# Kernel optimization log

Measured on AMD Instinct MI355X. Metric: run time of the kernel, lower is better.

The kernel has to match this reference:

```python
import jax, jax.numpy as jnp
import numpy as np

DIM_IN, DIM_K, DIM_V = 1024, 1024, 1024

def setup_inputs() -> dict:
    key = jax.random.key(0)
    k1, k2, k3, k4 = jax.random.split(key, 4)
    x = jax.random.normal(k1, (4, 2048, DIM_IN), dtype=jnp.float32)
    # Linear(dim_in, dim_k, bias=False): store as [in, out] for x @ W
    Wq = jax.random.normal(k2, (DIM_IN, DIM_K), dtype=jnp.float32) * (1.0 / np.sqrt(DIM_IN))
    Wk = jax.random.normal(k3, (DIM_IN, DIM_K), dtype=jnp.float32) * (1.0 / np.sqrt(DIM_IN))
    Wv = jax.random.normal(k4, (DIM_IN, DIM_V), dtype=jnp.float32) * (1.0 / np.sqrt(DIM_IN))
    return {"x": x, "Wq": Wq, "Wk": Wk, "Wv": Wv, "causal_mask": 1}

def reference(x, Wq, Wk, Wv, causal_mask):
    # x: [b, n, dim_in]
    b, n, _ = x.shape
    q = jnp.einsum('bnd,dk->bnk', x, Wq)
    k = jnp.einsum('bnd,dk->bnk', x, Wk)
    v = jnp.einsum('bnd,dv->bnv', x, Wv)
    scale = 1.0 / np.sqrt(Wq.shape[1])
    dist = jnp.einsum('bik,bjk->bij', q, k) * scale  # [b, n, n]
    if causal_mask:
        mask = jnp.tril(jnp.ones((n, n), dtype=bool))
        dist = jnp.where(mask, dist, -jnp.inf)
    attn = jax.nn.softmax(dist, axis=-1)
    return jnp.einsum('bij,bjv->biv', attn, v)  # [b, n, dim_v]
```

## Files before the change

kernel.cpp:

```cpp
#include <hip/hip_runtime.h>
#include <hip/hip_bf16.h>
#include <stdint.h>

#define BM 128
#define BN 128
#define BK 64

typedef __attribute__((ext_vector_type(8))) short bf16x8;
typedef __attribute__((ext_vector_type(4))) float floatx4;


__device__ __forceinline__ unsigned short f2bf(float f) {
    unsigned int x;
    __builtin_memcpy(&x, &f, 4);
    unsigned int r = (x + 0x7fffu + ((x >> 16) & 1u)) >> 16;
    return (unsigned short)r;
}

__device__ __forceinline__ float bf2f_hi(unsigned int u_hi_masked) {
    float f;
    __builtin_memcpy(&f, &u_hi_masked, 4);
    return f;
}

__device__ __forceinline__ void async_copy16(const void* g, void* l) {
    __builtin_amdgcn_global_load_lds(
        (const __attribute__((address_space(1))) void*)(uintptr_t)g,
        (__attribute__((address_space(3))) void*)(uint32_t)(uintptr_t)l,
        16, 0, 0);
}


__global__ __launch_bounds__(256) void prep(const float* __restrict__ x,
                                            const float* __restrict__ Wq,
                                            const float* __restrict__ Wk,
                                            const float* __restrict__ Wv,
                                            unsigned short* __restrict__ xb,
                                            unsigned short* __restrict__ wT) {
    __shared__ float tile[32][33];
    int bid = blockIdx.x;
    int tid = threadIdx.x;
    if (bid < 8192) {
        int i = bid * 256 + tid;
        float4 v = ((const float4*)x)[i];
        ushort4 o;
        o.x = f2bf(v.x);
        o.y = f2bf(v.y);
        o.z = f2bf(v.z);
        o.w = f2bf(v.w);
        ((ushort4*)xb)[i] = o;
    } else {
        int w = bid - 8192;
        int z = w >> 10;
        int r = w & 1023;
        int bx = (r & 31) * 32;
        int by = (r >> 5) * 32;
        const float* W = z == 0 ? Wq : (z == 1 ? Wk : Wv);
        int tx = tid & 31, ty = tid >> 5;
        for (int rr = 0; rr < 32; rr += 8)
            tile[ty + rr][tx] = W[(size_t)(by + ty + rr) * 1024 + bx + tx];
        __syncthreads();
        unsigned short* o = wT + (size_t)z * 1024 * 1024;
        for (int rr = 0; rr < 32; rr += 8)
            o[(size_t)(bx + ty + rr) * 1024 + by + tx] = f2bf(tile[tx][ty + rr]);
    }
}


__device__ __forceinline__ void gemm_core(const unsigned short* __restrict__ A,
                                          int lda,
                                          const unsigned short* __restrict__ B,
                                          int ldb, void* __restrict__ C,
                                          int ldc, bool out_bf16, int kend,
                                          float scale, int m0, int n0) {
    __shared__ __align__(16) unsigned short As[BM * BK];
    __shared__ __align__(16) unsigned short Bs[BN * BK];

    int tid = threadIdx.x;
    int lane = tid & 63;
    int wave = tid >> 6;
    int wm = (wave >> 1) * 64;
    int wn = (wave & 1) * 64;
    int fr = lane & 15;
    int kq = lane >> 4;

    floatx4 acc[4][4] = {};

    for (int k0 = 0; k0 < kend; k0 += BK) {
#pragma unroll
        for (int q = 0; q < 4; q++) {
            int c = tid + q * 256;
            int r = c >> 3, ko = (c & 7) * 8;
            async_copy16(A + (size_t)(m0 + r) * lda + k0 + ko, &As[c * 8]);
            async_copy16(B + (size_t)(n0 + r) * ldb + k0 + ko, &Bs[c * 8]);
        }
        __syncthreads();

#pragma unroll
        for (int kh = 0; kh < 2; kh++) {
            int kc = kh * 4 + kq;
            bf16x8 af[4], bfg[4];
#pragma unroll
            for (int mi = 0; mi < 4; mi++)
                af[mi] = *(const bf16x8*)&As[(wm + mi * 16 + fr) * BK + kc * 8];
#pragma unroll
            for (int ni = 0; ni < 4; ni++)
                bfg[ni] = *(const bf16x8*)&Bs[(wn + ni * 16 + fr) * BK + kc * 8];
#pragma unroll
            for (int mi = 0; mi < 4; mi++)
#pragma unroll
                for (int ni = 0; ni < 4; ni++)
                    acc[mi][ni] = __builtin_amdgcn_mfma_f32_16x16x32_bf16(
                        af[mi], bfg[ni], acc[mi][ni], 0, 0, 0);
        }
        __syncthreads();
    }

    int col0 = n0 + wn + fr;
    int rbase = m0 + wm + kq * 4;
    if (out_bf16) {
        unsigned short* Cb = (unsigned short*)C;
#pragma unroll
        for (int mi = 0; mi < 4; mi++)
#pragma unroll
            for (int ni = 0; ni < 4; ni++)
#pragma unroll
                for (int r = 0; r < 4; r++)
                    Cb[(size_t)(rbase + mi * 16 + r) * ldc + col0 + ni * 16] =
                        f2bf(acc[mi][ni][r] * scale);
    } else {
        float* Cb = (float*)C;
#pragma unroll
        for (int mi = 0; mi < 4; mi++)
#pragma unroll
            for (int ni = 0; ni < 4; ni++)
#pragma unroll
                for (int r = 0; r < 4; r++)
                    Cb[(size_t)(rbase + mi * 16 + r) * ldc + col0 + ni * 16] =
                        acc[mi][ni][r] * scale;
    }
}


__device__ __forceinline__ void tri_decode(int r2, int& mb, int& nb) {
    mb = (int)((sqrtf(8.0f * r2 + 1.0f) - 1.0f) * 0.5f);
    while ((mb + 1) * (mb + 2) / 2 <= r2) mb++;
    while (mb * (mb + 1) / 2 > r2) mb--;
    nb = r2 - mb * (mb + 1) / 2;
}


__global__ __launch_bounds__(256, 4) void gemm_qk(
    const unsigned short* __restrict__ xb, const unsigned short* __restrict__ wT,
    unsigned short* __restrict__ qk) {
    gemm_core(xb, 1024, wT, 1024, qk, 2048, true, 1024, 1.0f,
              blockIdx.y * BM, blockIdx.x * BN);
}


__global__ __launch_bounds__(256, 4) void gemm_s(
    const unsigned short* __restrict__ qk, unsigned short* __restrict__ S) {
    int bz = blockIdx.x / 136;
    int mb, nb;
    tri_decode(blockIdx.x - bz * 136, mb, nb);
    const unsigned short* Q = qk + (size_t)bz * 2048 * 2048;
    gemm_core(Q, 2048, Q + 1024, 2048, S + (size_t)bz * 2048 * 2048, 2048,
              true, 1024, 0.03125f, mb * BM, nb * BN);
}


__global__ __launch_bounds__(256, 4) void sm_vt(
    unsigned short* __restrict__ S, const unsigned short* __restrict__ wTv,
    const unsigned short* __restrict__ xb, unsigned short* __restrict__ vt) {
    int bid = blockIdx.x;
    if (bid < 512) {
        gemm_core(wTv, 1024, xb, 1024, vt, 8192, true, 1024, 1.0f,
                  (bid >> 6) * BM, (bid & 63) * BN);
        return;
    }
    int lane = threadIdx.x & 63;
    int row = (bid - 512) * 4 + (threadIdx.x >> 6);
    int i = row & 2047;
    unsigned short* s = S + (size_t)row * 2048;

    uint4 raw[4];
#pragma unroll
    for (int c = 0; c < 4; c++) raw[c] = ((const uint4*)s)[lane + c * 64];

    const float NEG = -1.0e30f;
    float p[32];
    float m = NEG;
#pragma unroll
    for (int c = 0; c < 4; c++) {
        const unsigned int* u = (const unsigned int*)&raw[c];
#pragma unroll
        for (int w = 0; w < 4; w++) {
            int j = c * 512 + lane * 8 + w * 2;
            float f0 = bf2f_hi(u[w] << 16);
            float f1 = bf2f_hi(u[w] & 0xffff0000u);
            f0 = (j <= i) ? f0 : NEG;
            f1 = (j + 1 <= i) ? f1 : NEG;
            p[c * 8 + w * 2] = f0;
            p[c * 8 + w * 2 + 1] = f1;
            m = fmaxf(m, fmaxf(f0, f1));
        }
    }
#pragma unroll
    for (int o = 32; o > 0; o >>= 1) m = fmaxf(m, __shfl_xor(m, o));

    float sum = 0.f;
#pragma unroll
    for (int t = 0; t < 32; t++) {
        p[t] = __expf(p[t] - m);
        sum += p[t];
    }
#pragma unroll
    for (int o = 32; o > 0; o >>= 1) sum += __shfl_xor(sum, o);
    float inv = 1.0f / sum;

#pragma unroll
    for (int c = 0; c < 4; c++) {
        uint4 out;
        unsigned int* u = (unsigned int*)&out;
#pragma unroll
        for (int w = 0; w < 4; w++) {
            unsigned int lo = f2bf(p[c * 8 + w * 2] * inv);
            unsigned int hi = f2bf(p[c * 8 + w * 2 + 1] * inv);
            u[w] = lo | (hi << 16);
        }
        ((uint4*)s)[lane + c * 64] = out;
    }
}


__global__ __launch_bounds__(256, 4) void gemm_pv(
    const unsigned short* __restrict__ S, const unsigned short* __restrict__ vt,
    float* __restrict__ out) {
    int b = blockIdx.x;
    int j = b < 256 ? b : 767 - b;
    int mb = j >> 5;
    int rem = j & 31;
    int bz = rem >> 3, nb = rem & 7;
    int kend = (mb + 1) * 128;
    gemm_core(S + (size_t)bz * 2048 * 2048, 2048, vt + (size_t)bz * 2048, 8192,
              out + (size_t)bz * 2048 * 1024, 1024, false, kend, 1.0f,
              mb * BM, nb * BN);
}


extern "C" void kernel_launch(void* const* d_in, const int* in_sizes, int n_in,
                              void* d_out, int out_size, void* d_ws,
                              size_t ws_size, hipStream_t stream) {
    const float* x = (const float*)d_in[0];
    const float* Wq = (const float*)d_in[1];
    const float* Wk = (const float*)d_in[2];
    const float* Wv = (const float*)d_in[3];

    char* ws = (char*)d_ws;
    unsigned short* qk = (unsigned short*)(ws);
    unsigned short* S = (unsigned short*)(ws + 33554432);
    unsigned short* vt = (unsigned short*)(ws + 67108864);
    unsigned short* xb = (unsigned short*)(ws + 83886080);
    unsigned short* wT = (unsigned short*)(ws + 100663296);

    prep<<<11264, 256, 0, stream>>>(x, Wq, Wk, Wv, xb, wT);
    gemm_qk<<<dim3(16, 64), 256, 0, stream>>>(xb, wT, qk);
    gemm_s<<<544, 256, 0, stream>>>(qk, S);
    sm_vt<<<2560, 256, 0, stream>>>(S, wT + 2 * 1024 * 1024, xb, vt);
    gemm_pv<<<512, 256, 0, stream>>>(S, vt, (float*)d_out);
}
```

Baseline: 250.7 us.

## Swizzle LDS tiles and double-buffer the PV GEMM k-loop

```diff
diff --git a/kernel.cpp b/kernel.cpp
--- a/kernel.cpp
+++ b/kernel.cpp
@@ -67,14 +67,15 @@
 }
 
 
-__device__ __forceinline__ void gemm_core(const unsigned short* __restrict__ A,
-                                          int lda,
-                                          const unsigned short* __restrict__ B,
-                                          int ldb, void* __restrict__ C,
-                                          int ldc, bool out_bf16, int kend,
-                                          float scale, int m0, int n0) {
-    __shared__ __align__(16) unsigned short As[BM * BK];
-    __shared__ __align__(16) unsigned short Bs[BN * BK];
+template <bool DBUF>
+__device__ __forceinline__ void gemm_core_t(const unsigned short* __restrict__ A,
+                                            int lda,
+                                            const unsigned short* __restrict__ B,
+                                            int ldb, void* __restrict__ C,
+                                            int ldc, bool out_bf16, int kend,
+                                            float scale, int m0, int n0) {
+    __shared__ __align__(16) unsigned short As[(DBUF ? 2 : 1) * BM * BK];
+    __shared__ __align__(16) unsigned short Bs[(DBUF ? 2 : 1) * BN * BK];
 
     int tid = threadIdx.x;
     int lane = tid & 63;
@@ -83,29 +84,36 @@
     int wn = (wave & 1) * 64;
     int fr = lane & 15;
     int kq = lane >> 4;
+    int frs = fr & 7;
+    int ko = (((tid & 7) ^ ((tid >> 3) & 7)) << 3);
 
     floatx4 acc[4][4] = {};
 
-    for (int k0 = 0; k0 < kend; k0 += BK) {
+    auto stage = [&](int buf, int k0) {
 #pragma unroll
         for (int q = 0; q < 4; q++) {
             int c = tid + q * 256;
-            int r = c >> 3, ko = (c & 7) * 8;
-            async_copy16(A + (size_t)(m0 + r) * lda + k0 + ko, &As[c * 8]);
-            async_copy16(B + (size_t)(n0 + r) * ldb + k0 + ko, &Bs[c * 8]);
-        }
-        __syncthreads();
-
+            int r = c >> 3;
+            async_copy16(A + (size_t)(m0 + r) * lda + k0 + ko,
+                         &As[buf * BM * BK + c * 8]);
+            async_copy16(B + (size_t)(n0 + r) * ldb + k0 + ko,
+                         &Bs[buf * BM * BK + c * 8]);
+        }
+    };
+
+    auto compute = [&](int buf) {
+        const unsigned short* as = &As[buf * BM * BK];
+        const unsigned short* bs = &Bs[buf * BM * BK];
 #pragma unroll
         for (int kh = 0; kh < 2; kh++) {
-            int kc = kh * 4 + kq;
+            int kcs = ((kh * 4 + kq) ^ frs) * 8;
             bf16x8 af[4], bfg[4];
 #pragma unroll
             for (int mi = 0; mi < 4; mi++)
-                af[mi] = *(const bf16x8*)&As[(wm + mi * 16 + fr) * BK + kc * 8];
+                af[mi] = *(const bf16x8*)&as[(wm + mi * 16 + fr) * BK + kcs];
 #pragma unroll
             for (int ni = 0; ni < 4; ni++)
-                bfg[ni] = *(const bf16x8*)&Bs[(wn + ni * 16 + fr) * BK + kc * 8];
+                bfg[ni] = *(const bf16x8*)&bs[(wn + ni * 16 + fr) * BK + kcs];
 #pragma unroll
             for (int mi = 0; mi < 4; mi++)
 #pragma unroll
@@ -113,7 +121,26 @@
                     acc[mi][ni] = __builtin_amdgcn_mfma_f32_16x16x32_bf16(
                         af[mi], bfg[ni], acc[mi][ni], 0, 0, 0);
         }
+    };
+
+    if (DBUF) {
+        stage(0, 0);
         __syncthreads();
+        int nt = kend / BK;
+        int cur = 0;
+        for (int t = 0; t < nt; t++) {
+            if (t + 1 < nt) stage(cur ^ 1, (t + 1) * BK);
+            compute(cur);
+            __syncthreads();
+            cur ^= 1;
+        }
+    } else {
+        for (int k0 = 0; k0 < kend; k0 += BK) {
+            stage(0, k0);
+            __syncthreads();
+            compute(0);
+            __syncthreads();
+        }
     }
 
     int col0 = n0 + wn + fr;
@@ -153,8 +180,8 @@
 __global__ __launch_bounds__(256, 4) void gemm_qk(
     const unsigned short* __restrict__ xb, const unsigned short* __restrict__ wT,
     unsigned short* __restrict__ qk) {
-    gemm_core(xb, 1024, wT, 1024, qk, 2048, true, 1024, 1.0f,
-              blockIdx.y * BM, blockIdx.x * BN);
+    gemm_core_t<false>(xb, 1024, wT, 1024, qk, 2048, true, 1024, 1.0f,
+                       blockIdx.y * BM, blockIdx.x * BN);
 }
 
 
@@ -164,8 +191,8 @@
     int mb, nb;
     tri_decode(blockIdx.x - bz * 136, mb, nb);
     const unsigned short* Q = qk + (size_t)bz * 2048 * 2048;
-    gemm_core(Q, 2048, Q + 1024, 2048, S + (size_t)bz * 2048 * 2048, 2048,
-              true, 1024, 0.03125f, mb * BM, nb * BN);
+    gemm_core_t<false>(Q, 2048, Q + 1024, 2048, S + (size_t)bz * 2048 * 2048,
+                       2048, true, 1024, 0.03125f, mb * BM, nb * BN);
 }
 
 
@@ -174,8 +201,8 @@
     const unsigned short* __restrict__ xb, unsigned short* __restrict__ vt) {
     int bid = blockIdx.x;
     if (bid < 512) {
-        gemm_core(wTv, 1024, xb, 1024, vt, 8192, true, 1024, 1.0f,
-                  (bid >> 6) * BM, (bid & 63) * BN);
+        gemm_core_t<false>(wTv, 1024, xb, 1024, vt, 8192, true, 1024, 1.0f,
+                           (bid >> 6) * BM, (bid & 63) * BN);
         return;
     }
     int lane = threadIdx.x & 63;
@@ -242,9 +269,10 @@
     int rem = j & 31;
     int bz = rem >> 3, nb = rem & 7;
     int kend = (mb + 1) * 128;
-    gemm_core(S + (size_t)bz * 2048 * 2048, 2048, vt + (size_t)bz * 2048, 8192,
-              out + (size_t)bz * 2048 * 1024, 1024, false, kend, 1.0f,
-              mb * BM, nb * BN);
+    gemm_core_t<true>(S + (size_t)bz * 2048 * 2048, 2048,
+                      vt + (size_t)bz * 2048, 8192,
+                      out + (size_t)bz * 2048 * 1024, 1024, false, kend, 1.0f,
+                      mb * BM, nb * BN);
 }
 
 
```

Result: slower. 313.2 us (+25.0%).
